# Kernel optimization log

Measured on AMD Instinct MI355X. Metric: run time of the kernel, lower is better.

The kernel has to match this reference:

```python
import jax, jax.numpy as jnp
import numpy as np

B, P, N, DIM = 2, 2, 1024, 256
HEADS, DH = 8, 64
INNER = HEADS * DH
HW = 32
C = HW * HW  # conv channels = h1*h2 = 1024
LN_EPS = 1e-5
BN_EPS = 1e-5


def setup_inputs() -> dict:
    key = jax.random.key(0)
    ks = jax.random.split(key, 10)
    return {
        "x": jax.random.normal(ks[0], (B, P, N, DIM), jnp.float32),
        "ln_g": jnp.ones((DIM,), jnp.float32),
        "ln_b": jnp.zeros((DIM,), jnp.float32),
        "w_qkv": jax.random.normal(ks[1], (DIM, 3 * INNER), jnp.float32) * DIM ** -0.5,
        "w_conv1": jax.random.normal(ks[2], (C, 2), jnp.float32) * 0.7,
        "w_conv2": jax.random.normal(ks[3], (C, 2), jnp.float32) * 0.7,
        "w_1x1": jax.random.normal(ks[4], (C, C), jnp.float32) * C ** -0.5,
        "bn_g": jnp.ones((C,), jnp.float32),
        "bn_b": jnp.zeros((C,), jnp.float32),
        "bn_m": jax.random.normal(ks[5], (C,), jnp.float32) * 0.1,
        "bn_v": jax.random.uniform(ks[6], (C,), jnp.float32, minval=0.5, maxval=1.5),
        "w_out": jax.random.normal(ks[7], (INNER, DIM), jnp.float32) * INNER ** -0.5,
        "b_out": jnp.zeros((DIM,), jnp.float32),
    }


def _dw_conv_w(a, w):
    # depthwise (1,2) kernel, reflection pad right by 1 (pad value = col W-2)
    ap = jnp.concatenate([a, a[..., -2:-1]], axis=-1)
    return ap[..., :-1] * w[:, 0][None, :, None, None] + ap[..., 1:] * w[:, 1][None, :, None, None]


def _dw_conv_h(a, w):
    # depthwise (2,1) kernel, reflection pad bottom by 1 (pad value = row H-2)
    ap = jnp.concatenate([a, a[:, :, -2:-1, :]], axis=2)
    return ap[:, :, :-1, :] * w[:, 0][None, :, None, None] + ap[:, :, 1:, :] * w[:, 1][None, :, None, None]


def reference(x, ln_g, ln_b, w_qkv, w_conv1, w_conv2, w_1x1, bn_g, bn_b, bn_m, bn_v, w_out, b_out):
    b, p, n, dim = x.shape
    # LayerNorm
    mu = jnp.mean(x, axis=-1, keepdims=True)
    var = jnp.mean(jnp.square(x - mu), axis=-1, keepdims=True)
    xn = (x - mu) * jax.lax.rsqrt(var + LN_EPS) * ln_g + ln_b
    # QKV projection, split heads
    qkv = xn @ w_qkv  # (b,p,n,3*inner)
    q, k, v = jnp.split(qkv, 3, axis=-1)
    split_heads = lambda t: t.reshape(b, p, n, HEADS, DH).transpose(0, 1, 3, 2, 4)
    q, k, v = map(split_heads, (q, k, v))  # (b,p,h,n,d)
    dots = jnp.einsum('bphnd,bphmd->bphnm', q, k) * (DH ** -0.5)  # (b,p,h,n,n)
    # rearrange scores: n=(h1 w1), m=(h2 w2) -> channels (h1 h2), spatial (w1 w2)
    a = dots.reshape(b, p, HEADS, HW, HW, HW, HW)
    a = a.transpose(0, 1, 2, 3, 5, 4, 6).reshape(b * p * HEADS, C, HW, HW)
    a = _dw_conv_w(a, w_conv1)
    a = _dw_conv_h(a, w_conv2)
    # 1x1 conv (no bias) + BatchNorm (inference) + SiLU
    a = jnp.einsum('bchw,oc->bohw', a, w_1x1)
    inv = jax.lax.rsqrt(bn_v + BN_EPS)
    a = (a - bn_m[None, :, None, None]) * (inv * bn_g)[None, :, None, None] + bn_b[None, :, None, None]
    a = a * jax.nn.sigmoid(a)
    # rearrange back to (b,p,h,n,n)
    a = a.reshape(b, p, HEADS, HW, HW, HW, HW).transpose(0, 1, 2, 3, 5, 4, 6).reshape(b, p, HEADS, n, n)
    attn = jax.nn.softmax(a, axis=-1)
    out = jnp.einsum('bphnm,bphmd->bphnd', attn, v)
    out = out.transpose(0, 1, 3, 2, 4).reshape(b, p, n, INNER)
    return out @ w_out + b_out
```

## Files before the change

### kernel.cpp

```cpp
#include <hip/hip_runtime.h>
#include <hip/hip_fp16.h>


#define DEV __device__ __forceinline__

typedef __attribute__((ext_vector_type(8))) _Float16 f16x8;
typedef __attribute__((ext_vector_type(4))) float f32x4;
typedef __attribute__((ext_vector_type(8))) unsigned short u16x8;

DEV float h2f_bits(unsigned short u) { __half h; *reinterpret_cast<unsigned short*>(&h) = u; return __half2float(h); }
DEV unsigned short f2h_bits(float f) { __half h = __float2half(f); return *reinterpret_cast<unsigned short*>(&h); }

__global__ __launch_bounds__(256) void prep_kernel(
    const float* __restrict__ wqkv, const float* __restrict__ w1x1,
    const float* __restrict__ wout,
    __half* __restrict__ WQKVT, __half* __restrict__ W1X1H, __half* __restrict__ WOTT) {
  int i0 = blockIdx.x * 256 + threadIdx.x;
  int stride = gridDim.x * 256;
  for (int i = i0; i < 1536 * 256; i += stride) {
    int j = i >> 8, k = i & 255;
    WQKVT[i] = __float2half(wqkv[k * 1536 + j]);
  }
  for (int i = i0; i < 1024 * 1024; i += stride) {
    int o = i >> 10, p = i & 1023;
    int blk = p >> 5, r = p & 31, a = r >> 3, bb = r & 7;
    int h1 = (blk >> 2) * 4 + a, h2 = (blk & 3) * 8 + bb;
    W1X1H[i] = __float2half(w1x1[o * 1024 + h1 * 32 + h2]);
  }
  for (int i = i0; i < 256 * 512; i += stride) {
    int j = i >> 9, k = i & 511;
    WOTT[i] = __float2half(wout[k * 256 + j]);
  }
}

__global__ __launch_bounds__(256) void ln_kernel(const float* __restrict__ x,
    const float* __restrict__ g, const float* __restrict__ b, __half* __restrict__ XN) {
  int row = blockIdx.x;
  int tid = threadIdx.x, lane = tid & 63, wid = tid >> 6;
  float xv = x[(size_t)row * 256 + tid];
  float s = xv, q = xv * xv;
#pragma unroll
  for (int off = 32; off; off >>= 1) { s += __shfl_xor(s, off); q += __shfl_xor(q, off); }
  __shared__ float rs[4], rq[4];
  if (lane == 0) { rs[wid] = s; rq[wid] = q; }
  __syncthreads();
  s = rs[0] + rs[1] + rs[2] + rs[3];
  q = rq[0] + rq[1] + rq[2] + rq[3];
  float mu = s * (1.f / 256.f);
  float var = q * (1.f / 256.f) - mu * mu;
  float r = rsqrtf(var + 1e-5f);
  XN[(size_t)row * 256 + tid] = __float2half((xv - mu) * r * g[tid] + b[tid]);
}

template <int BM, int BN, int BK, int WGN, int FM, int FN, class Epi>
__global__ __launch_bounds__(256) void gemm_bt(
    const __half* __restrict__ A, long long aStride,
    const __half* __restrict__ B, long long bStride,
    int K, Epi epi) {
  constexpr int CPR = BK / 8;
  constexpr int NCA = (BM * BK) / (8 * 256);
  constexpr int NCB = (BN * BK) / (8 * 256);
  constexpr int KSUB = BK / 32;
  __shared__ __align__(16) __half smA[2][BM * BK];
  __shared__ __align__(16) __half smB[2][BN * BK];
  const int tid = threadIdx.x;
  const int lane = tid & 63, wid = tid >> 6;
  const int wr = wid / WGN, wc = wid % WGN;
  const int gx = gridDim.x, gxy = gridDim.x * gridDim.y;
  const int nwg = gxy * gridDim.z;
  const int b_lin = blockIdx.x + blockIdx.y * gx + blockIdx.z * gxy;
  const int logical = (b_lin & 7) * (nwg >> 3) + (b_lin >> 3);
  const int bx = logical % gx, by = (logical / gx) % gridDim.y, bz = logical / gxy;
  const int img = bz;
  const int row0 = bx * BM;
  const int col0 = by * BN;
  const __half* Ab = A + (size_t)((long long)img * aStride);
  const __half* Bb = B + (size_t)((long long)img * bStride);
  f32x4 acc[FM][FN] = {};
  const int lr = lane & 15;
  const int kq = lane >> 4;

  auto swz = [](int c, int r) -> int {
    return (CPR == 8) ? (c ^ (r & 7)) : (c ^ ((r >> 1) & 3));
  };

  const __half* pA[NCA]; int dA[NCA];
  const __half* pB[NCB]; int dB[NCB];
#pragma unroll
  for (int it = 0; it < NCA; ++it) {
    int e = it * 256 + tid, r = e / CPR, c = e % CPR;
    pA[it] = Ab + (size_t)(row0 + r) * K + swz(c, r) * 8;
    dA[it] = r * BK + c * 8;
  }
#pragma unroll
  for (int it = 0; it < NCB; ++it) {
    int e = it * 256 + tid, r = e / CPR, c = e % CPR;
    pB[it] = Bb + (size_t)(col0 + r) * K + swz(c, r) * 8;
    dB[it] = r * BK + c * 8;
  }

  auto stage = [&](int buf, int kt) {
#pragma unroll
    for (int it = 0; it < NCA; ++it)
      __builtin_amdgcn_global_load_lds(
          (const __attribute__((address_space(1))) unsigned int*)(pA[it] + kt),
          (__attribute__((address_space(3))) unsigned int*)(&smA[buf][dA[it]]),
          16, 0, 0);
#pragma unroll
    for (int it = 0; it < NCB; ++it)
      __builtin_amdgcn_global_load_lds(
          (const __attribute__((address_space(1))) unsigned int*)(pB[it] + kt),
          (__attribute__((address_space(3))) unsigned int*)(&smB[buf][dB[it]]),
          16, 0, 0);
  };

  const int NT = K / BK;
  stage(0, 0);
  __syncthreads();
  int cur = 0;
  for (int t = 0; t < NT; ++t) {
    if (t + 1 < NT) stage(cur ^ 1, (t + 1) * BK);
#pragma unroll
    for (int kk = 0; kk < KSUB; ++kk) {
      f16x8 av[FM], bv[FN];
#pragma unroll
      for (int i = 0; i < FM; ++i) {
        int row = wr * FM * 16 + i * 16 + lr;
        int ch = swz(kk * 4 + kq, lr);
        av[i] = *reinterpret_cast<const f16x8*>(&smA[cur][row * BK + ch * 8]);
      }
#pragma unroll
      for (int j = 0; j < FN; ++j) {
        int row = wc * FN * 16 + j * 16 + lr;
        int ch = swz(kk * 4 + kq, lr);
        bv[j] = *reinterpret_cast<const f16x8*>(&smB[cur][row * BK + ch * 8]);
      }
#pragma unroll
      for (int i = 0; i < FM; ++i)
#pragma unroll
        for (int j = 0; j < FN; ++j)
          acc[i][j] = __builtin_amdgcn_mfma_f32_16x16x32_f16(av[i], bv[j], acc[i][j], 0, 0, 0);
    }
    __syncthreads();
    cur ^= 1;
  }

  const int orow = row0 + wr * FM * 16 + (lane >> 4) * 4;
  const int ocol = col0 + wc * FN * 16 + lr;
#pragma unroll
  for (int i = 0; i < FM; ++i)
#pragma unroll
    for (int j = 0; j < FN; ++j)
#pragma unroll
      for (int q = 0; q < 4; ++q)
        epi.store(img, orow + i * 16 + q, ocol + j * 16, acc[i][j][q]);
}

struct EpiQKV {
  __half *Q, *K, *V;
  DEV void store(int, int t, int j, float v) const {
    int part = j >> 9, inner = j & 511;
    int h = inner >> 6, d = inner & 63;
    int bp = t >> 10, n = t & 1023;
    size_t img = (size_t)(bp * 8 + h);
    if (part == 0)       Q[(img * 1024 + n) * 64 + d] = __float2half(v * 0.125f);
    else if (part == 1)  K[(img * 1024 + n) * 64 + d] = __float2half(v);
    else                 V[(img * 64 + d) * 1024 + n] = __float2half(v);
  }
};
struct EpiPV {
  __half* O;
  DEV void store(int img, int n, int d, float v) const {
    int bp = img >> 3, h = img & 7;
    O[((size_t)(bp * 1024 + n)) * 512 + h * 64 + d] = __float2half(v);
  }
};
struct EpiOut {
  float* out; const float* bias;
  DEV void store(int, int t, int j, float v) const {
    out[(size_t)t * 256 + j] = v + bias[j];
  }
};

__global__ __launch_bounds__(512) void qkconv_kernel(
    const __half* __restrict__ Q, const __half* __restrict__ Km,
    const float* __restrict__ wc1, const float* __restrict__ wc2,
    __half* __restrict__ AC) {
  constexpr int NP = 132;
  __shared__ __align__(16) char LDS[77824];
  __half* smA = (__half*)LDS;
  __half* smB = (__half*)(LDS + 16384);
  __half* Dt  = (__half*)LDS;
  __half* T   = (__half*)(LDS + 67584);
  const int tid = threadIdx.x;
  const int lane = tid & 63, wid = tid >> 6;
  const int wr = wid >> 2, wc = wid & 3;
  const int gx = gridDim.x, gxy = gx * gridDim.y;
  const int nwg = gxy * gridDim.z;
  const int b_lin = blockIdx.x + blockIdx.y * gx + blockIdx.z * gxy;
  const int logical = (b_lin & 7) * (nwg >> 3) + (b_lin >> 3);
  const int bx = logical % gx, by = (logical / gx) % gridDim.y, bz = logical / gxy;
  const int img = bz, row0 = bx * 128, col0 = by * 256;
  const __half* Qi = Q + ((size_t)img << 16);
  const __half* Ki = Km + ((size_t)img << 16);

#pragma unroll
  for (int it = 0; it < 2; ++it) {
    int e = it * 512 + tid, r = e >> 3, c = e & 7, sc = c ^ (r & 7);
    __builtin_amdgcn_global_load_lds(
        (const __attribute__((address_space(1))) unsigned int*)(Qi + (size_t)(row0 + r) * 64 + sc * 8),
        (__attribute__((address_space(3))) unsigned int*)(smA + r * 64 + c * 8), 16, 0, 0);
  }
#pragma unroll
  for (int it = 0; it < 4; ++it) {
    int e = it * 512 + tid, r = e >> 3, c = e & 7, sc = c ^ (r & 7);
    __builtin_amdgcn_global_load_lds(
        (const __attribute__((address_space(1))) unsigned int*)(Ki + (size_t)(col0 + r) * 64 + sc * 8),
        (__attribute__((address_space(3))) unsigned int*)(smB + r * 64 + c * 8), 16, 0, 0);
  }
  __syncthreads();

  const int lr = lane & 15, kq = lane >> 4;
  f32x4 acc[4][4] = {};
#pragma unroll
  for (int kk = 0; kk < 2; ++kk) {
    const int ch = (kk * 4 + kq) ^ (lr & 7);
    f16x8 av[4], bv[4];
#pragma unroll
    for (int i = 0; i < 4; ++i)
      av[i] = *reinterpret_cast<const f16x8*>(&smA[(wr * 64 + i * 16 + lr) * 64 + ch * 8]);
#pragma unroll
    for (int j = 0; j < 4; ++j)
      bv[j] = *reinterpret_cast<const f16x8*>(&smB[(wc * 64 + j * 16 + lr) * 64 + ch * 8]);
#pragma unroll
    for (int i = 0; i < 4; ++i)
#pragma unroll
      for (int j = 0; j < 4; ++j)
        acc[i][j] = __builtin_amdgcn_mfma_f32_16x16x32_f16(av[i], bv[j], acc[i][j], 0, 0, 0);
  }
  __syncthreads();

#pragma unroll
  for (int i = 0; i < 4; ++i) {
    int n0 = wr * 64 + i * 16 + kq * 4;
#pragma unroll
    for (int j = 0; j < 4; ++j) {
      int m = wc * 64 + j * 16 + lr;
      ushort4 o4;
      o4.x = f2h_bits(acc[i][j][0]); o4.y = f2h_bits(acc[i][j][1]);
      o4.z = f2h_bits(acc[i][j][2]); o4.w = f2h_bits(acc[i][j][3]);
      *reinterpret_cast<ushort4*>(Dt + m * NP + n0) = o4;
    }
  }
  __syncthreads();

  const int w2i = tid >> 7;
  const int b_  = (tid >> 4) & 7;
  const int a_  = (tid >> 2) & 3;
  const int w1q = (tid & 3) * 8;
  const int cch = (bx * 4 + a_) * 32 + (by * 8 + b_);
  const float u0 = wc1[2 * cch], u1 = wc1[2 * cch + 1];
  const float v0 = wc2[2 * cch], v1 = wc2[2 * cch + 1];
  const int cblk = (bx * 4 + by) * 32;
  __half* ACi = AC + ((size_t)img << 20);
  const int w1o = (tid >> 2) & 31, ck = tid & 3;

  for (int pass = 0; pass < 8; ++pass) {
    const int w2 = pass * 4 + w2i;
    const int w2n = (w2 < 31) ? w2 + 1 : 30;
    const __half* r0 = Dt + (b_ * 32 + w2) * NP + a_ * 32 + w1q;
    const __half* r1 = Dt + (b_ * 32 + w2n) * NP + a_ * 32 + w1q;
    float X[9];
    {
      ushort4 x0a = *reinterpret_cast<const ushort4*>(r0);
      ushort4 x0b = *reinterpret_cast<const ushort4*>(r0 + 4);
      ushort4 x1a = *reinterpret_cast<const ushort4*>(r1);
      ushort4 x1b = *reinterpret_cast<const ushort4*>(r1 + 4);
      X[0] = u0 * h2f_bits(x0a.x) + u1 * h2f_bits(x1a.x);
      X[1] = u0 * h2f_bits(x0a.y) + u1 * h2f_bits(x1a.y);
      X[2] = u0 * h2f_bits(x0a.z) + u1 * h2f_bits(x1a.z);
      X[3] = u0 * h2f_bits(x0a.w) + u1 * h2f_bits(x1a.w);
      X[4] = u0 * h2f_bits(x0b.x) + u1 * h2f_bits(x1b.x);
      X[5] = u0 * h2f_bits(x0b.y) + u1 * h2f_bits(x1b.y);
      X[6] = u0 * h2f_bits(x0b.z) + u1 * h2f_bits(x1b.z);
      X[7] = u0 * h2f_bits(x0b.w) + u1 * h2f_bits(x1b.w);
      X[8] = u0 * __half2float(r0[8]) + u1 * __half2float(r1[8]);
    }
#pragma unroll
    for (int k = 0; k < 8; ++k) {
      float ov = (w1q + k < 31) ? (v0 * X[k] + v1 * X[k + 1])
                                : (v0 * X[7] + v1 * X[6]);
      T[(w2i * 32 + w1q + k) * 40 + a_ * 8 + b_] = __float2half(ov);
    }
    __syncthreads();
    {
      const int w2o = pass * 4 + (tid >> 7);
      u16x8 v = *reinterpret_cast<const u16x8*>(T + ((tid >> 7) * 32 + w1o) * 40 + ck * 8);
      *reinterpret_cast<u16x8*>(ACi + (size_t)(w1o * 32 + w2o) * 1024 + cblk + ck * 8) = v;
    }
    __syncthreads();
  }
}

struct Epi1x1S {
  __half* P;
  const float *g, *b, *m, *vv;
  DEV void finalize(int img, int ob, int cb, int lane, f32x4 (&acc)[4][2]) const {
    const int lr = lane & 15, kq = lane >> 4;
    __half* Pi = P + ((size_t)img << 20);
#pragma unroll
    for (int ih = 0; ih < 2; ++ih) {
      float v[2][2][4];
      float mx = -1e30f;
#pragma unroll
      for (int di = 0; di < 2; ++di) {
        int i = ih * 2 + di;
#pragma unroll
        for (int q = 0; q < 4; ++q) {
          int o = ob + i * 16 + kq * 4 + q;
          float sc = rsqrtf(vv[o] + 1e-5f) * g[o];
          float mo = m[o], bo = b[o];
#pragma unroll
          for (int dj = 0; dj < 2; ++dj) {
            float t = (acc[i][dj][q] - mo) * sc + bo;
            t = t / (1.f + __expf(-t));
            v[di][dj][q] = t;
            mx = fmaxf(mx, t);
          }
        }
      }
#pragma unroll
      for (int off = 32; off; off >>= 1) mx = fmaxf(mx, __shfl_xor(mx, off));
      float sm = 0.f;
#pragma unroll
      for (int di = 0; di < 2; ++di)
#pragma unroll
        for (int dj = 0; dj < 2; ++dj)
#pragma unroll
          for (int q = 0; q < 4; ++q) {
            float e = __expf(v[di][dj][q] - mx);
            v[di][dj][q] = e; sm += e;
          }
#pragma unroll
      for (int off = 32; off; off >>= 1) sm += __shfl_xor(sm, off);
      float inv = 1.f / sm;
#pragma unroll
      for (int di = 0; di < 2; ++di) {
        int i = ih * 2 + di;
#pragma unroll
        for (int q = 0; q < 4; ++q) {
          int o = ob + i * 16 + kq * 4 + q;
          size_t nhi = (size_t)(o >> 5) * 32;
          int mlo = (o & 31) * 32;
#pragma unroll
          for (int dj = 0; dj < 2; ++dj) {
            int s = cb + dj * 16 + lr;
            Pi[(nhi + (s >> 5)) * 1024 + mlo + (s & 31)] = __float2half(v[di][dj][q] * inv);
          }
        }
      }
    }
  }
};

template <class Epi>
__global__ __launch_bounds__(512, 4) void gemm1x1(
    const __half* __restrict__ A,
    const __half* __restrict__ B, long long bStride,
    int K, Epi epi) {
  __shared__ __align__(16) __half smA[2][128 * 64];
  __shared__ __align__(16) __half smB[2][128 * 64];
  const int tid = threadIdx.x;
  const int lane = tid & 63, wid = tid >> 6;
  const int wr = wid >> 2, wc = wid & 3;
  const int gx = gridDim.x, gxy = gx * gridDim.y;
  const int nwg = gxy * gridDim.z;
  const int b_lin = blockIdx.x + blockIdx.y * gx + blockIdx.z * gxy;
  const int logical = (b_lin & 7) * (nwg >> 3) + (b_lin >> 3);
  const int bx = logical % gx, by = (logical / gx) % gridDim.y, bz = logical / gxy;
  const int img = bz, row0 = bx * 128, col0 = by * 128;
  const __half* Ab = A;
  const __half* Bb = B + (size_t)((long long)img * bStride);

  const __half* pA[2]; int dA[2];
  const __half* pB[2]; int dB[2];
#pragma unroll
  for (int it = 0; it < 2; ++it) {
    int e = it * 512 + tid, r = e >> 3, c = e & 7, sc = c ^ (r & 7);
    pA[it] = Ab + (size_t)(row0 + r) * K + sc * 8;
    pB[it] = Bb + (size_t)(col0 + r) * K + sc * 8;
    dA[it] = dB[it] = r * 64 + c * 8;
  }
  auto stage = [&](int buf, int kt) {
#pragma unroll
    for (int it = 0; it < 2; ++it)
      __builtin_amdgcn_global_load_lds(
          (const __attribute__((address_space(1))) unsigned int*)(pA[it] + kt),
          (__attribute__((address_space(3))) unsigned int*)(&smA[buf][dA[it]]),
          16, 0, 0);
#pragma unroll
    for (int it = 0; it < 2; ++it)
      __builtin_amdgcn_global_load_lds(
          (const __attribute__((address_space(1))) unsigned int*)(pB[it] + kt),
          (__attribute__((address_space(3))) unsigned int*)(&smB[buf][dB[it]]),
          16, 0, 0);
  };

  const int lr = lane & 15, kq = lane >> 4;
  f32x4 acc[4][2] = {};
  const int NT = K / 64;
  stage(0, 0);
  __syncthreads();
  int cur = 0;
  for (int t = 0; t < NT; ++t) {
    if (t + 1 < NT) stage(cur ^ 1, (t + 1) * 64);
#pragma unroll
    for (int kk = 0; kk < 2; ++kk) {
      const int ch = (kk * 4 + kq) ^ (lr & 7);
      f16x8 av[4], bv[2];
#pragma unroll
      for (int i = 0; i < 4; ++i)
        av[i] = *reinterpret_cast<const f16x8*>(&smA[cur][(wr * 64 + i * 16 + lr) * 64 + ch * 8]);
#pragma unroll
      for (int j = 0; j < 2; ++j)
        bv[j] = *reinterpret_cast<const f16x8*>(&smB[cur][(wc * 32 + j * 16 + lr) * 64 + ch * 8]);
      __builtin_amdgcn_s_setprio(1);
#pragma unroll
      for (int i = 0; i < 4; ++i)
#pragma unroll
        for (int j = 0; j < 2; ++j)
          acc[i][j] = __builtin_amdgcn_mfma_f32_16x16x32_f16(av[i], bv[j], acc[i][j], 0, 0, 0);
      __builtin_amdgcn_s_setprio(0);
    }
    __syncthreads();
    cur ^= 1;
  }
  epi.finalize(img, row0 + wr * 64, col0 + wc * 32, lane, acc);
}

extern "C" void kernel_launch(void* const* d_in, const int* in_sizes, int n_in,
                              void* d_out, int out_size, void* d_ws, size_t ws_size,
                              hipStream_t stream) {
  const float* x     = (const float*)d_in[0];
  const float* ln_g  = (const float*)d_in[1];
  const float* ln_b  = (const float*)d_in[2];
  const float* w_qkv = (const float*)d_in[3];
  const float* wc1   = (const float*)d_in[4];
  const float* wc2   = (const float*)d_in[5];
  const float* w1x1  = (const float*)d_in[6];
  const float* bn_g  = (const float*)d_in[7];
  const float* bn_b  = (const float*)d_in[8];
  const float* bn_m  = (const float*)d_in[9];
  const float* bn_v  = (const float*)d_in[10];
  const float* w_out = (const float*)d_in[11];
  const float* b_out = (const float*)d_in[12];
  float* out = (float*)d_out;

  const size_t MB = 1024 * 1024;
  char* ws = (char*)d_ws;
  __half* Pb = (__half*)ws;
  __half* ACb = (__half*)(ws + 64 * MB);
  char* p = ws + 128 * MB;
  __half* XN    = (__half*)p; p += 2 * MB;
  __half* WQKVT = (__half*)p; p += 1536 * 256 * 2;
  __half* W1X1H = (__half*)p; p += 2 * MB;
  __half* WOTT  = (__half*)p; p += 256 * 512 * 2;
  __half* Qb    = (__half*)p; p += 4 * MB;
  __half* Kb    = (__half*)p; p += 4 * MB;
  __half* Vtb   = (__half*)p; p += 4 * MB;
  __half* Ob    = (__half*)p; p += 4 * MB;

  prep_kernel<<<2048, 256, 0, stream>>>(w_qkv, w1x1, w_out, WQKVT, W1X1H, WOTT);
  ln_kernel<<<4096, 256, 0, stream>>>(x, ln_g, ln_b, XN);

  { EpiQKV e{Qb, Kb, Vtb};
    gemm_bt<128, 128, 64, 2, 4, 4, EpiQKV><<<dim3(32, 12, 1), 256, 0, stream>>>(
        XN, 0, WQKVT, 0, 256, e); }

  qkconv_kernel<<<dim3(8, 4, 32), 512, 0, stream>>>(Qb, Kb, wc1, wc2, ACb);

  { Epi1x1S e{Pb, bn_g, bn_b, bn_m, bn_v};
    gemm1x1<Epi1x1S><<<dim3(8, 8, 32), 512, 0, stream>>>(
        W1X1H, ACb, 1 << 20, 1024, e); }

  { EpiPV e{Ob};
    gemm_bt<64, 64, 64, 2, 2, 2, EpiPV><<<dim3(16, 1, 32), 256, 0, stream>>>(
        Pb, 1 << 20, Vtb, 65536, 1024, e); }

  { EpiOut e{out, b_out};
    gemm_bt<64, 64, 64, 2, 2, 2, EpiOut><<<dim3(64, 4, 1), 256, 0, stream>>>(
        Ob, 0, WOTT, 0, 512, e); }
}
```

Before: 184.5 us.

## Enlarge 1x1-conv GEMM tile to 256x128 with K=32 stages and retile PV GEMM

The 1x1 conv GEMM now uses a 256x128 block tile with each of 8 waves computing a 64x64 sub-tile (4x4 MFMAs) over K-steps of 32, using a new 4-chunk LDS swizzle. The fused BN/SiLU/softmax epilogue is extended to handle the wider per-wave output. This raises arithmetic intensity per LDS load and halves the grid. The PV GEMM also switches to a 128x64 tile. The cost is more accumulator registers per thread, which may lower occupancy under the 512x4 launch bounds, plus twice as many barrier iterations.

Result: slower. 188.7 us (+2.3%).

```diff
diff --git a/kernel.cpp b/kernel.cpp
--- a/kernel.cpp
+++ b/kernel.cpp
@@ -302,60 +302,63 @@
   }
 }
 
-struct Epi1x1S {
+struct Epi1x1F {
   __half* P;
   const float *g, *b, *m, *vv;
-  DEV void finalize(int img, int ob, int cb, int lane, f32x4 (&acc)[4][2]) const {
+  DEV void finalize(int img, int ob, int cb, int lane, f32x4 (&acc)[4][4]) const {
     const int lr = lane & 15, kq = lane >> 4;
     __half* Pi = P + ((size_t)img << 20);
 #pragma unroll
     for (int ih = 0; ih < 2; ++ih) {
-      float v[2][2][4];
-      float mx = -1e30f;
-#pragma unroll
-      for (int di = 0; di < 2; ++di) {
-        int i = ih * 2 + di;
-#pragma unroll
-        for (int q = 0; q < 4; ++q) {
-          int o = ob + i * 16 + kq * 4 + q;
-          float sc = rsqrtf(vv[o] + 1e-5f) * g[o];
-          float mo = m[o], bo = b[o];
-#pragma unroll
-          for (int dj = 0; dj < 2; ++dj) {
-            float t = (acc[i][dj][q] - mo) * sc + bo;
-            t = t / (1.f + __expf(-t));
-            v[di][dj][q] = t;
-            mx = fmaxf(mx, t);
+#pragma unroll
+      for (int sh = 0; sh < 2; ++sh) {
+        float v[2][2][4];
+        float mx = -1e30f;
+#pragma unroll
+        for (int di = 0; di < 2; ++di) {
+          int i = ih * 2 + di;
+#pragma unroll
+          for (int q = 0; q < 4; ++q) {
+            int o = ob + i * 16 + kq * 4 + q;
+            float sc = rsqrtf(vv[o] + 1e-5f) * g[o];
+            float mo = m[o], bo = b[o];
+#pragma unroll
+            for (int dj = 0; dj < 2; ++dj) {
+              float t = (acc[i][sh * 2 + dj][q] - mo) * sc + bo;
+              t = t / (1.f + __expf(-t));
+              v[di][dj][q] = t;
+              mx = fmaxf(mx, t);
+            }
           }
         }
-      }
-#pragma unroll
-      for (int off = 32; off; off >>= 1) mx = fmaxf(mx, __shfl_xor(mx, off));
-      float sm = 0.f;
-#pragma unroll
-      for (int di = 0; di < 2; ++di)
-#pragma unroll
-        for (int dj = 0; dj < 2; ++dj)
+#pragma unroll
+        for (int off = 32; off; off >>= 1) mx = fmaxf(mx, __shfl_xor(mx, off));
+        float sm = 0.f;
+#pragma unroll
+        for (int di = 0; di < 2; ++di)
+#pragma unroll
+          for (int dj = 0; dj < 2; ++dj)
+#pragma unroll
+            for (int q = 0; q < 4; ++q) {
+              float e = __expf(v[di][dj][q] - mx);
+              v[di][dj][q] = e; sm += e;
+            }
+#pragma unroll
+        for (int off = 32; off; off >>= 1) sm += __shfl_xor(sm, off);
+        float inv = 1.f / sm;
+#pragma unroll
+        for (int di = 0; di < 2; ++di) {
+          int i = ih * 2 + di;
 #pragma unroll
           for (int q = 0; q < 4; ++q) {
-            float e = __expf(v[di][dj][q] - mx);
-            v[di][dj][q] = e; sm += e;
-          }
-#pragma unroll
-      for (int off = 32; off; off >>= 1) sm += __shfl_xor(sm, off);
-      float inv = 1.f / sm;
-#pragma unroll
-      for (int di = 0; di < 2; ++di) {
-        int i = ih * 2 + di;
-#pragma unroll
-        for (int q = 0; q < 4; ++q) {
-          int o = ob + i * 16 + kq * 4 + q;
-          size_t nhi = (size_t)(o >> 5) * 32;
-          int mlo = (o & 31) * 32;
-#pragma unroll
-          for (int dj = 0; dj < 2; ++dj) {
-            int s = cb + dj * 16 + lr;
-            Pi[(nhi + (s >> 5)) * 1024 + mlo + (s & 31)] = __float2half(v[di][dj][q] * inv);
+            int o = ob + i * 16 + kq * 4 + q;
+            size_t nhi = (size_t)(o >> 5) * 32;
+            int mlo = (o & 31) * 32;
+#pragma unroll
+            for (int dj = 0; dj < 2; ++dj) {
+              int s = cb + (sh * 2 + dj) * 16 + lr;
+              Pi[(nhi + (s >> 5)) * 1024 + mlo + (s & 31)] = __float2half(v[di][dj][q] * inv);
+            }
           }
         }
       }
@@ -368,28 +371,32 @@
     const __half* __restrict__ A,
     const __half* __restrict__ B, long long bStride,
     int K, Epi epi) {
-  __shared__ __align__(16) __half smA[2][128 * 64];
-  __shared__ __align__(16) __half smB[2][128 * 64];
+  __shared__ __align__(16) __half smA[2][256 * 32];
+  __shared__ __align__(16) __half smB[2][128 * 32];
   const int tid = threadIdx.x;
   const int lane = tid & 63, wid = tid >> 6;
-  const int wr = wid >> 2, wc = wid & 3;
+  const int wr = wid >> 1, wc = wid & 1;
   const int gx = gridDim.x, gxy = gx * gridDim.y;
   const int nwg = gxy * gridDim.z;
   const int b_lin = blockIdx.x + blockIdx.y * gx + blockIdx.z * gxy;
   const int logical = (b_lin & 7) * (nwg >> 3) + (b_lin >> 3);
   const int bx = logical % gx, by = (logical / gx) % gridDim.y, bz = logical / gxy;
-  const int img = bz, row0 = bx * 128, col0 = by * 128;
+  const int img = bz, row0 = bx * 256, col0 = by * 128;
   const __half* Ab = A;
   const __half* Bb = B + (size_t)((long long)img * bStride);
 
   const __half* pA[2]; int dA[2];
-  const __half* pB[2]; int dB[2];
 #pragma unroll
   for (int it = 0; it < 2; ++it) {
-    int e = it * 512 + tid, r = e >> 3, c = e & 7, sc = c ^ (r & 7);
+    int e = it * 512 + tid, r = e >> 2, c = e & 3, sc = c ^ ((r >> 1) & 3);
     pA[it] = Ab + (size_t)(row0 + r) * K + sc * 8;
-    pB[it] = Bb + (size_t)(col0 + r) * K + sc * 8;
-    dA[it] = dB[it] = r * 64 + c * 8;
+    dA[it] = r * 32 + c * 8;
+  }
+  const __half* pB1; int dB1;
+  {
+    int r = tid >> 2, c = tid & 3, sc = c ^ ((r >> 1) & 3);
+    pB1 = Bb + (size_t)(col0 + r) * K + sc * 8;
+    dB1 = r * 32 + c * 8;
   }
   auto stage = [&](int buf, int kt) {
 #pragma unroll
@@ -398,44 +405,42 @@
           (const __attribute__((address_space(1))) unsigned int*)(pA[it] + kt),
           (__attribute__((address_space(3))) unsigned int*)(&smA[buf][dA[it]]),
           16, 0, 0);
-#pragma unroll
-    for (int it = 0; it < 2; ++it)
-      __builtin_amdgcn_global_load_lds(
-          (const __attribute__((address_space(1))) unsigned int*)(pB[it] + kt),
-          (__attribute__((address_space(3))) unsigned int*)(&smB[buf][dB[it]]),
-          16, 0, 0);
+    __builtin_amdgcn_global_load_lds(
+        (const __attribute__((address_space(1))) unsigned int*)(pB1 + kt),
+        (__attribute__((address_space(3))) unsigned int*)(&smB[buf][dB1]),
+        16, 0, 0);
   };
 
   const int lr = lane & 15, kq = lane >> 4;
-  f32x4 acc[4][2] = {};
-  const int NT = K / 64;
+  const int ch = kq ^ ((lr >> 1) & 3);
+  const int aOff = (wr * 64 + lr) * 32 + ch * 8;
+  const int bOff = (wc * 64 + lr) * 32 + ch * 8;
+  f32x4 acc[4][4] = {};
+
+  const int NT = K / 32;
   stage(0, 0);
   __syncthreads();
   int cur = 0;
   for (int t = 0; t < NT; ++t) {
-    if (t + 1 < NT) stage(cur ^ 1, (t + 1) * 64);
-#pragma unroll
-    for (int kk = 0; kk < 2; ++kk) {
-      const int ch = (kk * 4 + kq) ^ (lr & 7);
-      f16x8 av[4], bv[2];
-#pragma unroll
-      for (int i = 0; i < 4; ++i)
-        av[i] = *reinterpret_cast<const f16x8*>(&smA[cur][(wr * 64 + i * 16 + lr) * 64 + ch * 8]);
-#pragma unroll
-      for (int j = 0; j < 2; ++j)
-        bv[j] = *reinterpret_cast<const f16x8*>(&smB[cur][(wc * 32 + j * 16 + lr) * 64 + ch * 8]);
-      __builtin_amdgcn_s_setprio(1);
-#pragma unroll
-      for (int i = 0; i < 4; ++i)
-#pragma unroll
-        for (int j = 0; j < 2; ++j)
-          acc[i][j] = __builtin_amdgcn_mfma_f32_16x16x32_f16(av[i], bv[j], acc[i][j], 0, 0, 0);
-      __builtin_amdgcn_s_setprio(0);
-    }
+    if (t + 1 < NT) stage(cur ^ 1, (t + 1) * 32);
+    f16x8 av[4], bv[4];
+#pragma unroll
+    for (int i = 0; i < 4; ++i)
+      av[i] = *reinterpret_cast<const f16x8*>(&smA[cur][aOff + i * 512]);
+#pragma unroll
+    for (int j = 0; j < 4; ++j)
+      bv[j] = *reinterpret_cast<const f16x8*>(&smB[cur][bOff + j * 512]);
+    __builtin_amdgcn_s_setprio(1);
+#pragma unroll
+    for (int i = 0; i < 4; ++i)
+#pragma unroll
+      for (int j = 0; j < 4; ++j)
+        acc[i][j] = __builtin_amdgcn_mfma_f32_16x16x32_f16(av[i], bv[j], acc[i][j], 0, 0, 0);
+    __builtin_amdgcn_s_setprio(0);
     __syncthreads();
     cur ^= 1;
   }
-  epi.finalize(img, row0 + wr * 64, col0 + wc * 32, lane, acc);
+  epi.finalize(img, row0 + wr * 64, col0 + wc * 64, lane, acc);
 }
 
 extern "C" void kernel_launch(void* const* d_in, const int* in_sizes, int n_in,
@@ -479,12 +484,12 @@
 
   qkconv_kernel<<<dim3(8, 4, 32), 512, 0, stream>>>(Qb, Kb, wc1, wc2, ACb);
 
-  { Epi1x1S e{Pb, bn_g, bn_b, bn_m, bn_v};
-    gemm1x1<Epi1x1S><<<dim3(8, 8, 32), 512, 0, stream>>>(
+  { Epi1x1F e{Pb, bn_g, bn_b, bn_m, bn_v};
+    gemm1x1<Epi1x1F><<<dim3(4, 8, 32), 512, 0, stream>>>(
         W1X1H, ACb, 1 << 20, 1024, e); }
 
   { EpiPV e{Ob};
-    gemm_bt<64, 64, 64, 2, 2, 2, EpiPV><<<dim3(16, 1, 32), 256, 0, stream>>>(
+    gemm_bt<128, 64, 64, 2, 4, 2, EpiPV><<<dim3(8, 1, 32), 256, 0, stream>>>(
         Pb, 1 << 20, Vtb, 65536, 1024, e); }
 
   { EpiOut e{out, b_out};
```
